# Kernel tuning notes

Measured on AMD Instinct MI355X. Metric: run time of the kernel, lower is better.

Reference implementation:

```python
import jax, jax.numpy as jnp
import numpy as np

DIM = 3072      # model dim (Qwen-Image)
HEADS = 24
HD = 128        # head dim; inner = HEADS*HD = 3072
INNER = HEADS * HD
FF = 4 * DIM    # 12288
S_IMG = 1024
S_TXT = 256
S_TOT = S_IMG + S_TXT
B = 1
EPS = 1e-6
SCALE_SHIFT = 1.0


def setup_inputs() -> dict:
    key = jax.random.key(0)
    ks = iter(jax.random.split(key, 64))
    W = 0.02

    def nrm(shape, s=W):
        return jax.random.normal(next(ks), shape, dtype=jnp.float32) * s

    # RoPE tables for the joint (txt first, then img) sequence, interleaved layout
    pos = jnp.arange(S_TOT, dtype=jnp.float32)
    inv = 1.0 / (10000.0 ** (jnp.arange(HD // 2, dtype=jnp.float32) / (HD // 2)))
    ang = pos[:, None] * inv[None, :]                       # [S, HD/2]
    rope_cos = jnp.repeat(jnp.cos(ang), 2, axis=-1)         # [S, HD]
    rope_sin = jnp.repeat(jnp.sin(ang), 2, axis=-1)

    inp = {
        "hidden_states": jax.random.normal(next(ks), (B, S_IMG, DIM), dtype=jnp.float32),
        "encoder_hidden_states": jax.random.normal(next(ks), (B, S_TXT, DIM), dtype=jnp.float32),
        "temb": jax.random.normal(next(ks), (B, DIM), dtype=jnp.float32),
        "rope_cos": rope_cos,
        "rope_sin": rope_sin,
        # modulation (AWQW4A16Linear equivalent)
        "img_mod_w": nrm((6 * DIM, DIM)), "img_mod_b": nrm((6 * DIM,)),
        "txt_mod_w": nrm((6 * DIM, DIM)), "txt_mod_b": nrm((6 * DIM,)),
        # attention (SVDQW4A4Linear equivalents)
        "qkv_w": nrm((3 * INNER, DIM)), "qkv_b": nrm((3 * INNER,)),
        "add_qkv_w": nrm((3 * INNER, DIM)), "add_qkv_b": nrm((3 * INNER,)),
        "norm_q_g": jnp.ones((HD,), jnp.float32), "norm_k_g": jnp.ones((HD,), jnp.float32),
        "norm_added_q_g": jnp.ones((HD,), jnp.float32), "norm_added_k_g": jnp.ones((HD,), jnp.float32),
        "to_out_w": nrm((DIM, INNER)), "to_out_b": nrm((DIM,)),
        "to_add_out_w": nrm((DIM, INNER)), "to_add_out_b": nrm((DIM,)),
        # MLPs
        "img_mlp_w1": nrm((FF, DIM)), "img_mlp_b1": nrm((FF,)),
        "img_mlp_w2": nrm((DIM, FF)), "img_mlp_b2": nrm((DIM,)),
        "txt_mlp_w1": nrm((FF, DIM)), "txt_mlp_b1": nrm((FF,)),
        "txt_mlp_w2": nrm((DIM, FF)), "txt_mlp_b2": nrm((DIM,)),
    }
    return inp


def _lin(x, w, b):
    return jnp.matmul(x, w.T) + b


def _ln(x):  # LayerNorm, no affine, eps=1e-6
    mu = jnp.mean(x, axis=-1, keepdims=True)
    var = jnp.mean(jnp.square(x - mu), axis=-1, keepdims=True)
    return (x - mu) * jax.lax.rsqrt(var + EPS)


def _rms(x, g):  # per-head RMSNorm over last dim (HD)
    ms = jnp.mean(jnp.square(x), axis=-1, keepdims=True)
    return x * jax.lax.rsqrt(ms + EPS) * g


def _rope(x, cos, sin):  # x: [B,S,H,D], cos/sin: [S,D], interleaved rotate
    x1 = x[..., 0::2]
    x2 = x[..., 1::2]
    xr = jnp.stack([-x2, x1], axis=-1).reshape(x.shape)
    return x * cos[None, :, None, :] + xr * sin[None, :, None, :]


def _reorder_mod(m):
    # view(B,-1,6).transpose(1,2).reshape(B,-1): de-interleave 6 modulation vecs
    b = m.shape[0]
    return m.reshape(b, DIM, 6).transpose(0, 2, 1).reshape(b, 6 * DIM)


def _modulate(x, mod):
    shift, scale, gate = jnp.split(mod, 3, axis=-1)
    return x * (scale + SCALE_SHIFT)[:, None, :] + shift[:, None, :], gate[:, None, :]


def _mlp(x, w1, b1, w2, b2):  # GELU(tanh) MLP
    h = jax.nn.gelu(_lin(x, w1, b1), approximate=True)
    return _lin(h, w2, b2)


def reference(hidden_states, encoder_hidden_states, temb, rope_cos, rope_sin,
              img_mod_w, img_mod_b, txt_mod_w, txt_mod_b,
              qkv_w, qkv_b, add_qkv_w, add_qkv_b,
              norm_q_g, norm_k_g, norm_added_q_g, norm_added_k_g,
              to_out_w, to_out_b, to_add_out_w, to_add_out_b,
              img_mlp_w1, img_mlp_b1, img_mlp_w2, img_mlp_b2,
              txt_mlp_w1, txt_mlp_b1, txt_mlp_w2, txt_mlp_b2):
    b = hidden_states.shape[0]

    img_mod = _reorder_mod(_lin(jax.nn.silu(temb), img_mod_w, img_mod_b))
    txt_mod = _reorder_mod(_lin(jax.nn.silu(temb), txt_mod_w, txt_mod_b))
    img_mod1, img_mod2 = jnp.split(img_mod, 2, axis=-1)
    txt_mod1, txt_mod2 = jnp.split(txt_mod, 2, axis=-1)

    img_modulated, img_gate1 = _modulate(_ln(hidden_states), img_mod1)
    txt_modulated, txt_gate1 = _modulate(_ln(encoder_hidden_states), txt_mod1)

    # ---- joint attention ----
    img_q, img_k, img_v = jnp.split(_lin(img_modulated, qkv_w, qkv_b), 3, axis=-1)
    txt_q, txt_k, txt_v = jnp.split(_lin(txt_modulated, add_qkv_w, add_qkv_b), 3, axis=-1)

    def heads(x):  # [B,S,INNER] -> [B,S,H,HD]
        return x.reshape(b, x.shape[1], HEADS, HD)

    img_q = _rms(heads(img_q), norm_q_g)
    img_k = _rms(heads(img_k), norm_k_g)
    txt_q = _rms(heads(txt_q), norm_added_q_g)
    txt_k = _rms(heads(txt_k), norm_added_k_g)

    q = jnp.concatenate([txt_q, img_q], axis=1)  # txt first
    k = jnp.concatenate([txt_k, img_k], axis=1)
    v = jnp.concatenate([heads(txt_v), heads(img_v)], axis=1)

    q = _rope(q, rope_cos, rope_sin)
    k = _rope(k, rope_cos, rope_sin)

    scale = 1.0 / jnp.sqrt(jnp.float32(HD))
    scores = jnp.einsum('bqhd,bkhd->bhqk', q, k) * scale
    probs = jax.nn.softmax(scores, axis=-1)
    attn = jnp.einsum('bhqk,bkhd->bqhd', probs, v).reshape(b, S_TOT, INNER)

    txt_attn = attn[:, :S_TXT, :]
    img_attn = attn[:, S_TXT:, :]
    img_attn = _lin(img_attn, to_out_w, to_out_b)
    txt_attn = _lin(txt_attn, to_add_out_w, to_add_out_b)

    hidden_states = hidden_states + img_gate1 * img_attn
    encoder_hidden_states = encoder_hidden_states + txt_gate1 * txt_attn

    # ---- MLPs ----
    img_m2, img_gate2 = _modulate(_ln(hidden_states), img_mod2)
    hidden_states = hidden_states + img_gate2 * _mlp(img_m2, img_mlp_w1, img_mlp_b1, img_mlp_w2, img_mlp_b2)

    txt_m2, txt_gate2 = _modulate(_ln(encoder_hidden_states), txt_mod2)
    encoder_hidden_states = encoder_hidden_states + txt_gate2 * _mlp(txt_m2, txt_mlp_w1, txt_mlp_b1, txt_mlp_w2, txt_mlp_b2)

    return (encoder_hidden_states, hidden_states)
```

## Files before the change

### kernel.cpp

```cpp
#include <hip/hip_runtime.h>

#define DIMC   3072
#define HEADS  24
#define HD     128
#define FF     12288
#define S_IMG  1024
#define S_TXT  256
#define S_TOT  1280
#define EPSF   1e-6f

typedef __attribute__((ext_vector_type(8))) short bf16x8;
typedef __attribute__((ext_vector_type(4))) float f32x4;
typedef __attribute__((ext_vector_type(4))) float float4v;
typedef __attribute__((ext_vector_type(4))) unsigned int u32x4;

__device__ __forceinline__ unsigned short f2bf(float f) {
    union { float f; unsigned u; } c; c.f = f;
    unsigned u = c.u;
    unsigned r = (u + 0x7fffu + ((u >> 16) & 1u)) >> 16;
    return (unsigned short)r;
}
__device__ __forceinline__ float b2f(unsigned short h) {
    union { unsigned u; float f; } c; c.u = ((unsigned)h) << 16;
    return c.f;
}
__device__ __forceinline__ unsigned packbf(float a, float b) {
    union { float f; unsigned u; } x, y; x.f = a; y.f = b;
    return __builtin_amdgcn_perm(y.u + 0x8000u, x.u + 0x8000u, 0x07060302);
}
__device__ __forceinline__ float gelu_tanh(float v) {
    float u = 1.5957691216057308f * (v + 0.044715f * v * v * v);
    float e = __expf(u);
    float t = 1.0f - 2.0f / (e + 1.0f);
    return 0.5f * v * (1.0f + t);
}

#define GLL16(gsrc, ldst)                                                     \
    __builtin_amdgcn_global_load_lds(                                         \
        (const __attribute__((address_space(1))) void*)(gsrc),                \
        (__attribute__((address_space(3))) void*)(ldst), 16, 0, 0)

struct GemmArgs {
    const unsigned short* A;
    const void* B;
    const float* bias;
    void* out;
    const float* base;
    const float* gate;
};

__device__ __forceinline__ void epi_store(int EPI, const GemmArgs& g,
                                          float v, long o, int) {
}

template<int EPI>
__global__ __launch_bounds__(512, 2)
void gemm_big(GemmArgs g0, GemmArgs g1, int ysplit,
              int K, int lda, int ldb, int ldout)
{
    __shared__ __align__(16) char smem[131072];
    char* smemA = smem;
    char* smemB = smem + 65536;

    const int tid  = threadIdx.x;
    const int lane = tid & 63;
    const int wave = tid >> 6;
    const int wm = wave >> 2, wc = wave & 3;

    const int by = blockIdx.y;
    const bool second = (by >= ysplit);
    const GemmArgs g = second ? g1 : g0;
    const int bm = (second ? by - ysplit : by) * 256;
    const int bn = blockIdx.x * 256;

    const unsigned short* A = g.A;
    const float* Bf = (const float*)g.B;

    const int rA = lane >> 3;
    const int cA = (lane & 7) ^ rA;
    const int pB = tid & 7;
    const int rB0 = tid >> 3;
    const int swB = (rB0 & 7) << 4;

    float4v breg[4][2];

    auto BLOAD = [&](int t) {
        const float* src = Bf + (long)t * 64 + pB * 8;
        #pragma unroll
        for (int i = 0; i < 4; i++) {
            const float* p = src + (long)(bn + rB0 + i * 64) * ldb;
            breg[i][0] = *(const float4v*)p;
            breg[i][1] = *(const float4v*)(p + 4);
        }
    };
    auto ASTAGE = [&](int buf, int t) {
        const long kof = (long)t * 64 + cA * 8;
        #pragma unroll
        for (int i = 0; i < 4; i++) {
            int r = i * 64 + wave * 8 + rA;
            GLL16(A + (long)(bm + r) * lda + kof,
                  smemA + buf * 32768 + i * 8192 + wave * 1024);
        }
    };
    auto BSTORE = [&](int buf) {
        #pragma unroll
        for (int i = 0; i < 4; i++) {
            int r = rB0 + i * 64;
            u32x4 w;
            w[0] = packbf(breg[i][0][0], breg[i][0][1]);
            w[1] = packbf(breg[i][0][2], breg[i][0][3]);
            w[2] = packbf(breg[i][1][0], breg[i][1][1]);
            w[3] = packbf(breg[i][1][2], breg[i][1][3]);
            *(u32x4*)(smemB + buf * 32768 + r * 128 + ((pB * 16) ^ swB)) = w;
        }
    };

    f32x4 acc[8][4] = {};
    auto COMPUTE = [&](int buf) {
        #pragma unroll
        for (int ks = 0; ks < 2; ks++) {
            const int kb = ks * 64 + (lane >> 4) * 16;
            bf16x8 af[8], bfr[4];
            #pragma unroll
            for (int mi = 0; mi < 8; mi++) {
                int r = wm * 128 + mi * 16 + (lane & 15);
                af[mi] = *(const bf16x8*)(smemA + buf * 32768 + r * 128 + (kb ^ ((r & 7) << 4)));
            }
            #pragma unroll
            for (int ni = 0; ni < 4; ni++) {
                int r = wc * 64 + ni * 16 + (lane & 15);
                bfr[ni] = *(const bf16x8*)(smemB + buf * 32768 + r * 128 + (kb ^ ((r & 7) << 4)));
            }
            #pragma unroll
            for (int mi = 0; mi < 8; mi++)
                #pragma unroll
                for (int ni = 0; ni < 4; ni++)
                    acc[mi][ni] = __builtin_amdgcn_mfma_f32_16x16x32_bf16(
                        af[mi], bfr[ni], acc[mi][ni], 0, 0, 0);
        }
    };

    const int nk = K >> 6;
    BLOAD(0);
    ASTAGE(0, 0);
    BSTORE(0);
    __syncthreads();
    for (int t = 0; t < nk; ++t) {
        const int cur = t & 1;
        if (t + 1 < nk) {
            BLOAD(t + 1);
            ASTAGE(cur ^ 1, t + 1);
        }
        __builtin_amdgcn_sched_barrier(0);
        COMPUTE(cur);
        __builtin_amdgcn_sched_barrier(0);
        if (t + 1 < nk) BSTORE(cur ^ 1);
        __syncthreads();
    }

    unsigned short* outh = (unsigned short*)g.out;
    float*          outf = (float*)g.out;
    #pragma unroll
    for (int mi = 0; mi < 8; mi++) {
        #pragma unroll
        for (int ni = 0; ni < 4; ni++) {
            int n = bn + wc * 64 + ni * 16 + (lane & 15);
            float bv = g.bias ? g.bias[n] : 0.0f;
            #pragma unroll
            for (int r = 0; r < 4; r++) {
                int m = bm + wm * 128 + mi * 16 + (lane >> 4) * 4 + r;
                float v = acc[mi][ni][r] + bv;
                long o = (long)m * ldout + n;
                if constexpr (EPI == 0) outf[o] = v;
                else                    outh[o] = f2bf(gelu_tanh(v));
            }
        }
    }
}

template<int EPI, bool BF16B>
__global__ __launch_bounds__(256)
void gemm_bt(GemmArgs g0, GemmArgs g1, int ysplit,
             int K, int lda, int ldb, int ldout,
             long batchA, long batchB, long batchOut)
{
    __shared__ __align__(16) char smem[65536];
    char* smemA = smem;
    char* smemB = smem + 32768;

    const int tid  = threadIdx.x;
    const int lane = tid & 63;
    const int wave = tid >> 6;
    const int wm = wave >> 1, wc = wave & 1;

    const int by = blockIdx.y;
    const bool second = (by >= ysplit);
    const GemmArgs g = second ? g1 : g0;
    const int bm = (second ? by - ysplit : by) * 128;
    const int bn = blockIdx.x * 128;

    const unsigned short* A = g.A + (long)blockIdx.z * batchA;
    const float* Bf = (const float*)g.B + (long)blockIdx.z * batchB;
    const unsigned short* Bh = (const unsigned short*)g.B + (long)blockIdx.z * batchB;

    const int rA = lane >> 3;
    const int cA = (lane & 7) ^ rA;
    const int pB = tid & 7;
    const int rB0 = tid >> 3;
    const int swB = (rB0 & 7) << 4;

    float4v breg[4][2];

    auto BLOAD = [&](int t) {
        const float* src = Bf + (long)t * 64 + pB * 8;
        #pragma unroll
        for (int i = 0; i < 4; i++) {
            const float* p = src + (long)(bn + rB0 + i * 32) * ldb;
            breg[i][0] = *(const float4v*)p;
            breg[i][1] = *(const float4v*)(p + 4);
        }
    };
    auto STAGE_A = [&](int buf, int t) {
        const long kof = (long)t * 64 + cA * 8;
        #pragma unroll
        for (int i = 0; i < 4; i++) {
            int r = i * 32 + wave * 8 + rA;
            GLL16(A + (long)(bm + r) * lda + kof,
                  smemA + buf * 16384 + i * 4096 + wave * 1024);
        }
    };
    auto STAGE_B16 = [&](int buf, int t) {
        const long kof = (long)t * 64 + cA * 8;
        #pragma unroll
        for (int i = 0; i < 4; i++) {
            int r = i * 32 + wave * 8 + rA;
            GLL16(Bh + (long)(bn + r) * ldb + kof,
                  smemB + buf * 16384 + i * 4096 + wave * 1024);
        }
    };
    auto BSTORE = [&](int buf) {
        #pragma unroll
        for (int i = 0; i < 4; i++) {
            int r = rB0 + i * 32;
            u32x4 w;
            w[0] = packbf(breg[i][0][0], breg[i][0][1]);
            w[1] = packbf(breg[i][0][2], breg[i][0][3]);
            w[2] = packbf(breg[i][1][0], breg[i][1][1]);
            w[3] = packbf(breg[i][1][2], breg[i][1][3]);
            *(u32x4*)(smemB + buf * 16384 + r * 128 + ((pB * 16) ^ swB)) = w;
        }
    };

    f32x4 acc[4][4] = {};
    auto COMPUTE = [&](int buf) {
        #pragma unroll
        for (int ks = 0; ks < 2; ks++) {
            const int kb = ks * 64 + (lane >> 4) * 16;
            bf16x8 af[4], bfr[4];
            #pragma unroll
            for (int mi = 0; mi < 4; mi++) {
                int r = wm * 64 + mi * 16 + (lane & 15);
                af[mi] = *(const bf16x8*)(smemA + buf * 16384 + r * 128 + (kb ^ ((r & 7) << 4)));
            }
            #pragma unroll
            for (int ni = 0; ni < 4; ni++) {
                int r = wc * 64 + ni * 16 + (lane & 15);
                bfr[ni] = *(const bf16x8*)(smemB + buf * 16384 + r * 128 + (kb ^ ((r & 7) << 4)));
            }
            #pragma unroll
            for (int mi = 0; mi < 4; mi++)
                #pragma unroll
                for (int ni = 0; ni < 4; ni++)
                    acc[mi][ni] = __builtin_amdgcn_mfma_f32_16x16x32_bf16(
                        af[mi], bfr[ni], acc[mi][ni], 0, 0, 0);
        }
    };

    const int nk = K >> 6;
    if constexpr (BF16B) {
        STAGE_A(0, 0); STAGE_B16(0, 0);
    } else {
        BLOAD(0); STAGE_A(0, 0); BSTORE(0);
    }
    __syncthreads();
    for (int t = 0; t < nk; ++t) {
        const int cur = t & 1;
        if (t + 1 < nk) {
            if constexpr (BF16B) {
                STAGE_A(cur ^ 1, t + 1); STAGE_B16(cur ^ 1, t + 1);
            } else {
                BLOAD(t + 1); STAGE_A(cur ^ 1, t + 1);
            }
        }
        __builtin_amdgcn_sched_barrier(0);
        COMPUTE(cur);
        __builtin_amdgcn_sched_barrier(0);
        if constexpr (!BF16B) { if (t + 1 < nk) BSTORE(cur ^ 1); }
        __syncthreads();
    }

    unsigned short* outh = (unsigned short*)g.out + (long)blockIdx.z * batchOut;
    float*          outf = (float*)g.out + (long)blockIdx.z * batchOut;
    #pragma unroll
    for (int mi = 0; mi < 4; mi++) {
        #pragma unroll
        for (int ni = 0; ni < 4; ni++) {
            int n = bn + wc * 64 + ni * 16 + (lane & 15);
            float bv = g.bias ? g.bias[n] : 0.0f;
            #pragma unroll
            for (int r = 0; r < 4; r++) {
                int m = bm + wm * 64 + mi * 16 + (lane >> 4) * 4 + r;
                float v = acc[mi][ni][r] + bv;
                long o = (long)m * ldout + n;
                if constexpr (EPI == 0)      outf[o] = v;
                else if constexpr (EPI == 1) outh[o] = f2bf(v);
                else if constexpr (EPI == 2) outh[o] = f2bf(gelu_tanh(v));
                else                         outf[o] = g.base[o] + g.gate[n] * v;
            }
        }
    }
}

__global__ void silu_k(const float* __restrict__ x, float* __restrict__ out) {
    int i = blockIdx.x * 256 + threadIdx.x;
    if (i < DIMC) { float v = x[i]; out[i] = v / (1.0f + expf(-v)); }
}

__global__ __launch_bounds__(256)
void mod_gemv(const float* __restrict__ st,
              const float* __restrict__ Wimg, const float* __restrict__ bimg,
              const float* __restrict__ Wtxt, const float* __restrict__ btxt,
              float* __restrict__ mimg, float* __restrict__ mtxt)
{
    int wv = threadIdx.x >> 6, lane = threadIdx.x & 63;
    int r = blockIdx.x * 4 + wv;
    const float* W = blockIdx.y ? Wtxt : Wimg;
    const float* b = blockIdx.y ? btxt : bimg;
    float* out = blockIdx.y ? mtxt : mimg;
    const float* row = W + (long)r * DIMC;
    float acc = 0.f;
    #pragma unroll
    for (int j = 0; j < 12; j++) {
        float4v wvv = ((const float4v*)row)[lane + j * 64];
        float4v xv  = ((const float4v*)st)[lane + j * 64];
        acc += wvv[0] * xv[0] + wvv[1] * xv[1] + wvv[2] * xv[2] + wvv[3] * xv[3];
    }
    #pragma unroll
    for (int o = 32; o; o >>= 1) acc += __shfl_xor(acc, o);
    if (lane == 0) {
        int d = r / 6, j6 = r % 6;
        out[j6 * DIMC + d] = acc + b[r];
    }
}

__global__ __launch_bounds__(256)
void ln_mod(const float* __restrict__ x, const float* __restrict__ shift,
            const float* __restrict__ scale, unsigned short* __restrict__ out)
{
    __shared__ float red[8];
    long row = blockIdx.x;
    const float* xr = x + row * DIMC;
    float4v v[3];
    float sum = 0.f, sq = 0.f;
    #pragma unroll
    for (int j = 0; j < 3; j++) {
        v[j] = ((const float4v*)xr)[threadIdx.x + j * 256];
        #pragma unroll
        for (int c = 0; c < 4; c++) { sum += v[j][c]; sq += v[j][c] * v[j][c]; }
    }
    int lane = threadIdx.x & 63, wv = threadIdx.x >> 6;
    #pragma unroll
    for (int o = 32; o; o >>= 1) { sum += __shfl_xor(sum, o); sq += __shfl_xor(sq, o); }
    if (lane == 0) { red[wv] = sum; red[4 + wv] = sq; }
    __syncthreads();
    sum = red[0] + red[1] + red[2] + red[3];
    sq  = red[4] + red[5] + red[6] + red[7];
    float mu = sum / DIMC;
    float var = sq / DIMC - mu * mu;
    float rstd = rsqrtf(var + EPSF);
    #pragma unroll
    for (int j = 0; j < 3; j++) {
        int nb = (threadIdx.x + j * 256) * 4;
        #pragma unroll
        for (int c = 0; c < 4; c++) {
            int n = nb + c;
            float y = (v[j][c] - mu) * rstd * (scale[n] + 1.0f) + shift[n];
            out[row * DIMC + n] = f2bf(y);
        }
    }
}

__global__ __launch_bounds__(64)
void qkv_post(const float* __restrict__ qkv_img, const float* __restrict__ qkv_txt,
              const float* __restrict__ nqg, const float* __restrict__ nkg,
              const float* __restrict__ naqg, const float* __restrict__ nakg,
              const float* __restrict__ rc, const float* __restrict__ rs,
              unsigned short* __restrict__ q, unsigned short* __restrict__ k,
              unsigned short* __restrict__ vt)
{
    int s = blockIdx.x;
    int h = blockIdx.y;
    int d0 = threadIdx.x;
    const float *src, *gq, *gk;
    if (s < S_TXT) { src = qkv_txt + (long)s * 3 * DIMC; gq = naqg; gk = nakg; }
    else           { src = qkv_img + (long)(s - S_TXT) * 3 * DIMC; gq = nqg; gk = nkg; }

    float q0 = src[h * HD + d0],            q1 = src[h * HD + d0 + 64];
    float k0 = src[DIMC + h * HD + d0],     k1 = src[DIMC + h * HD + d0 + 64];
    float v0 = src[2 * DIMC + h * HD + d0], v1 = src[2 * DIMC + h * HD + d0 + 64];

    float sqq = q0 * q0 + q1 * q1;
    float sqk = k0 * k0 + k1 * k1;
    #pragma unroll
    for (int o = 32; o; o >>= 1) { sqq += __shfl_xor(sqq, o); sqk += __shfl_xor(sqk, o); }
    float rq = rsqrtf(sqq / (float)HD + EPSF);
    float rk = rsqrtf(sqk / (float)HD + EPSF);
    q0 *= rq * gq[d0]; q1 *= rq * gq[d0 + 64];
    k0 *= rk * gk[d0]; k1 *= rk * gk[d0 + 64];

    float qp0 = __shfl_xor(q0, 1), qp1 = __shfl_xor(q1, 1);
    float kp0 = __shfl_xor(k0, 1), kp1 = __shfl_xor(k1, 1);
    float c0 = rc[(long)s * HD + d0], c1 = rc[(long)s * HD + d0 + 64];
    float s0 = rs[(long)s * HD + d0], s1 = rs[(long)s * HD + d0 + 64];
    float sgn = (d0 & 1) ? 1.0f : -1.0f;
    float qo0 = q0 * c0 + sgn * qp0 * s0;
    float qo1 = q1 * c1 + sgn * qp1 * s1;
    float ko0 = k0 * c0 + sgn * kp0 * s0;
    float ko1 = k1 * c1 + sgn * kp1 * s1;

    const float scl = 0.08838834764831845f;
    long qkbase = ((long)h * S_TOT + s) * HD;
    q[qkbase + d0]      = f2bf(qo0 * scl);
    q[qkbase + d0 + 64] = f2bf(qo1 * scl);
    k[qkbase + d0]      = f2bf(ko0);
    k[qkbase + d0 + 64] = f2bf(ko1);
    vt[((long)h * HD + d0) * S_TOT + s]        = f2bf(v0);
    vt[((long)h * HD + d0 + 64) * S_TOT + s]   = f2bf(v1);
}

__global__ __launch_bounds__(256)
void softmax_k(unsigned short* __restrict__ scores)
{
    long row = (long)blockIdx.x * 4 + (threadIdx.x >> 6);
    int lane = threadIdx.x & 63;
    unsigned short* p = scores + row * S_TOT;
    float v[20];
    float mx = -1e30f;
    #pragma unroll
    for (int j = 0; j < 20; j++) { v[j] = b2f(p[lane + j * 64]); mx = fmaxf(mx, v[j]); }
    #pragma unroll
    for (int o = 32; o; o >>= 1) mx = fmaxf(mx, __shfl_xor(mx, o));
    float sum = 0.f;
    #pragma unroll
    for (int j = 0; j < 20; j++) { v[j] = __expf(v[j] - mx); sum += v[j]; }
    #pragma unroll
    for (int o = 32; o; o >>= 1) sum += __shfl_xor(sum, o);
    float inv = 1.0f / sum;
    #pragma unroll
    for (int j = 0; j < 20; j++) p[lane + j * 64] = f2bf(v[j] * inv);
}

extern "C" void kernel_launch(void* const* d_in, const int* in_sizes, int n_in,
                              void* d_out, int out_size, void* d_ws, size_t ws_size,
                              hipStream_t stream)
{
    const float* hidden   = (const float*)d_in[0];
    const float* enc      = (const float*)d_in[1];
    const float* temb     = (const float*)d_in[2];
    const float* rope_cos = (const float*)d_in[3];
    const float* rope_sin = (const float*)d_in[4];
    const float* img_mod_w = (const float*)d_in[5];
    const float* img_mod_b = (const float*)d_in[6];
    const float* txt_mod_w = (const float*)d_in[7];
    const float* txt_mod_b = (const float*)d_in[8];
    const float* qkv_w     = (const float*)d_in[9];
    const float* qkv_b     = (const float*)d_in[10];
    const float* add_qkv_w = (const float*)d_in[11];
    const float* add_qkv_b = (const float*)d_in[12];
    const float* norm_q_g  = (const float*)d_in[13];
    const float* norm_k_g  = (const float*)d_in[14];
    const float* norm_aq_g = (const float*)d_in[15];
    const float* norm_ak_g = (const float*)d_in[16];
    const float* to_out_w  = (const float*)d_in[17];
    const float* to_out_b  = (const float*)d_in[18];
    const float* to_add_out_w = (const float*)d_in[19];
    const float* to_add_out_b = (const float*)d_in[20];
    const float* img_mlp_w1 = (const float*)d_in[21];
    const float* img_mlp_b1 = (const float*)d_in[22];
    const float* img_mlp_w2 = (const float*)d_in[23];
    const float* img_mlp_b2 = (const float*)d_in[24];
    const float* txt_mlp_w1 = (const float*)d_in[25];
    const float* txt_mlp_b1 = (const float*)d_in[26];
    const float* txt_mlp_w2 = (const float*)d_in[27];
    const float* txt_mlp_b2 = (const float*)d_in[28];

    char* w = (char*)d_ws;
    auto alloc = [&](size_t bytes) { char* p = w; w += (bytes + 255) & ~(size_t)255; return p; };
    float* silu_t  = (float*)alloc(DIMC * 4);
    float* mod_img = (float*)alloc(6 * DIMC * 4);
    float* mod_txt = (float*)alloc(6 * DIMC * 4);
    unsigned short* mA_img = (unsigned short*)alloc((long)S_IMG * DIMC * 2);
    unsigned short* mA_txt = (unsigned short*)alloc((long)S_TXT * DIMC * 2);
    float* qkv_img = (float*)alloc((long)S_IMG * 3 * DIMC * 4);
    float* qkv_txt = (float*)alloc((long)S_TXT * 3 * DIMC * 4);
    unsigned short* qb = (unsigned short*)alloc((long)HEADS * S_TOT * HD * 2);
    unsigned short* kb = (unsigned short*)alloc((long)HEADS * S_TOT * HD * 2);
    unsigned short* vt = (unsigned short*)alloc((long)HEADS * HD * S_TOT * 2);
    unsigned short* scores = (unsigned short*)alloc((long)HEADS * S_TOT * S_TOT * 2);
    unsigned short* attn = (unsigned short*)alloc((long)S_TOT * DIMC * 2);
    float* h1_img = (float*)alloc((long)S_IMG * DIMC * 4);
    float* h1_txt = (float*)alloc((long)S_TXT * DIMC * 4);
    unsigned short* gelu_img = (unsigned short*)alloc((long)S_IMG * FF * 2);
    unsigned short* gelu_txt = (unsigned short*)alloc((long)S_TXT * FF * 2);

    float* out_enc = (float*)d_out;
    float* out_hid = (float*)d_out + (long)S_TXT * DIMC;

    silu_k<<<12, 256, 0, stream>>>(temb, silu_t);
    mod_gemv<<<dim3(4608, 2), 256, 0, stream>>>(silu_t, img_mod_w, img_mod_b,
                                                txt_mod_w, txt_mod_b, mod_img, mod_txt);

    ln_mod<<<S_IMG, 256, 0, stream>>>(hidden, mod_img, mod_img + DIMC, mA_img);
    ln_mod<<<S_TXT, 256, 0, stream>>>(enc, mod_txt, mod_txt + DIMC, mA_txt);

    {
        GemmArgs gi{mA_img, qkv_w, qkv_b, qkv_img, nullptr, nullptr};
        GemmArgs gt{mA_txt, add_qkv_w, add_qkv_b, qkv_txt, nullptr, nullptr};
        gemm_big<0><<<dim3(36, 5), 512, 0, stream>>>(
            gi, gt, 4, DIMC, DIMC, DIMC, 3 * DIMC);
    }

    qkv_post<<<dim3(S_TOT, HEADS), 64, 0, stream>>>(
        qkv_img, qkv_txt, norm_q_g, norm_k_g, norm_aq_g, norm_ak_g,
        rope_cos, rope_sin, qb, kb, vt);

    {
        GemmArgs gs{qb, kb, nullptr, scores, nullptr, nullptr};
        gemm_bt<1, true><<<dim3(10, 10, HEADS), 256, 0, stream>>>(
            gs, gs, 10, HD, HD, HD, S_TOT,
            (long)S_TOT * HD, (long)S_TOT * HD, (long)S_TOT * S_TOT);
    }
    softmax_k<<<(HEADS * S_TOT) / 4, 256, 0, stream>>>(scores);
    {
        GemmArgs gp{scores, vt, nullptr, attn, nullptr, nullptr};
        gemm_bt<1, true><<<dim3(1, 10, HEADS), 256, 0, stream>>>(
            gp, gp, 10, S_TOT, S_TOT, S_TOT, DIMC,
            (long)S_TOT * S_TOT, (long)HD * S_TOT, HD);
    }

    {
        GemmArgs gi{attn + (long)S_TXT * DIMC, to_out_w, to_out_b, h1_img, hidden, mod_img + 2 * DIMC};
        GemmArgs gt{attn, to_add_out_w, to_add_out_b, h1_txt, enc, mod_txt + 2 * DIMC};
        gemm_bt<3, false><<<dim3(24, 10), 256, 0, stream>>>(
            gi, gt, 8, DIMC, DIMC, DIMC, DIMC, 0, 0, 0);
    }

    ln_mod<<<S_IMG, 256, 0, stream>>>(h1_img, mod_img + 3 * DIMC, mod_img + 4 * DIMC, mA_img);
    ln_mod<<<S_TXT, 256, 0, stream>>>(h1_txt, mod_txt + 3 * DIMC, mod_txt + 4 * DIMC, mA_txt);

    {
        GemmArgs gi{mA_img, img_mlp_w1, img_mlp_b1, gelu_img, nullptr, nullptr};
        GemmArgs gt{mA_txt, txt_mlp_w1, txt_mlp_b1, gelu_txt, nullptr, nullptr};
        gemm_big<2><<<dim3(48, 5), 512, 0, stream>>>(
            gi, gt, 4, DIMC, DIMC, DIMC, FF);
    }
    {
        GemmArgs gi{gelu_img, img_mlp_w2, img_mlp_b2, out_hid, h1_img, mod_img + 5 * DIMC};
        GemmArgs gt{gelu_txt, txt_mlp_w2, txt_mlp_b2, out_enc, h1_txt, mod_txt + 5 * DIMC};
        gemm_bt<3, false><<<dim3(24, 10), 256, 0, stream>>>(
            gi, gt, 8, FF, FF, FF, DIMC, 0, 0, 0);
    }
}
```

Baseline: 863.6 us.

## Split-K the output and MLP-down GEMMs, fuse reduction with residual and LayerNorm

The to_out and MLP-down GEMMs, which ran on only 240 workgroups, are now split along K (2-way and 4-way) using the blockIdx.z batch dimension. Each split writes fp32 partials into the reused scores buffer. New reduce_ln and reduce_out kernels sum the partials and apply bias, gate and residual; reduce_ln also performs the following LayerNorm and modulation, which replaces the separate ln_mod launches. The aim is better GPU occupancy on the narrow GEMMs, at the cost of extra partial-buffer traffic.

```diff
diff --git a/kernel.cpp b/kernel.cpp
--- a/kernel.cpp
+++ b/kernel.cpp
@@ -45,13 +45,8 @@
     const void* B;
     const float* bias;
     void* out;
-    const float* base;
-    const float* gate;
+    long bOut;
 };
-
-__device__ __forceinline__ void epi_store(int EPI, const GemmArgs& g,
-                                          float v, long o, int) {
-}
 
 template<int EPI>
 __global__ __launch_bounds__(512, 2)
@@ -182,7 +177,7 @@
 __global__ __launch_bounds__(256)
 void gemm_bt(GemmArgs g0, GemmArgs g1, int ysplit,
              int K, int lda, int ldb, int ldout,
-             long batchA, long batchB, long batchOut)
+             long batchA, long batchB)
 {
     __shared__ __align__(16) char smem[65536];
     char* smemA = smem;
@@ -299,8 +294,8 @@
         __syncthreads();
     }
 
-    unsigned short* outh = (unsigned short*)g.out + (long)blockIdx.z * batchOut;
-    float*          outf = (float*)g.out + (long)blockIdx.z * batchOut;
+    unsigned short* outh = (unsigned short*)g.out + (long)blockIdx.z * g.bOut;
+    float*          outf = (float*)g.out + (long)blockIdx.z * g.bOut;
     #pragma unroll
     for (int mi = 0; mi < 4; mi++) {
         #pragma unroll
@@ -313,9 +308,7 @@
                 float v = acc[mi][ni][r] + bv;
                 long o = (long)m * ldout + n;
                 if constexpr (EPI == 0)      outf[o] = v;
-                else if constexpr (EPI == 1) outh[o] = f2bf(v);
-                else if constexpr (EPI == 2) outh[o] = f2bf(gelu_tanh(v));
-                else                         outf[o] = g.base[o] + g.gate[n] * v;
+                else                         outh[o] = f2bf(v);
             }
         }
     }
@@ -388,6 +381,75 @@
             out[row * DIMC + n] = f2bf(y);
         }
     }
+}
+
+__global__ __launch_bounds__(256)
+void reduce_ln(const float* __restrict__ p0, const float* __restrict__ p1,
+               const float* __restrict__ pbias, const float* __restrict__ base,
+               const float* __restrict__ gate1, const float* __restrict__ shift2,
+               const float* __restrict__ scale2,
+               float* __restrict__ h1, unsigned short* __restrict__ mA)
+{
+    __shared__ float red[8];
+    long off = (long)blockIdx.x * DIMC;
+    float4v v[3];
+    float sum = 0.f, sq = 0.f;
+    #pragma unroll
+    for (int j = 0; j < 3; j++) {
+        int idx = threadIdx.x + j * 256;
+        float4v a  = ((const float4v*)(base + off))[idx];
+        float4v q0 = ((const float4v*)(p0 + off))[idx];
+        float4v q1 = ((const float4v*)(p1 + off))[idx];
+        float4v gb = ((const float4v*)pbias)[idx];
+        float4v gt = ((const float4v*)gate1)[idx];
+        #pragma unroll
+        for (int c = 0; c < 4; c++) {
+            float val = a[c] + gt[c] * (gb[c] + q0[c] + q1[c]);
+            v[j][c] = val; sum += val; sq += val * val;
+        }
+        ((float4v*)(h1 + off))[idx] = v[j];
+    }
+    int lane = threadIdx.x & 63, wv = threadIdx.x >> 6;
+    #pragma unroll
+    for (int o = 32; o; o >>= 1) { sum += __shfl_xor(sum, o); sq += __shfl_xor(sq, o); }
+    if (lane == 0) { red[wv] = sum; red[4 + wv] = sq; }
+    __syncthreads();
+    sum = red[0] + red[1] + red[2] + red[3];
+    sq  = red[4] + red[5] + red[6] + red[7];
+    float mu = sum / DIMC;
+    float rstd = rsqrtf(sq / DIMC - mu * mu + EPSF);
+    #pragma unroll
+    for (int j = 0; j < 3; j++) {
+        int nb = (threadIdx.x + j * 256) * 4;
+        #pragma unroll
+        for (int c = 0; c < 4; c++) {
+            int n = nb + c;
+            float y = (v[j][c] - mu) * rstd * (scale2[n] + 1.0f) + shift2[n];
+            mA[off + n] = f2bf(y);
+        }
+    }
+}
+
+__global__ __launch_bounds__(256)
+void reduce_out(const float* __restrict__ p, long PS,
+                const float* __restrict__ h1, const float* __restrict__ wbias,
+                const float* __restrict__ gate2, float* __restrict__ out, int n4)
+{
+    int i = blockIdx.x * 256 + threadIdx.x;
+    if (i >= n4) return;
+    int n = (i * 4) % DIMC;
+    float4v s = ((const float4v*)p)[i];
+    float4v s1 = ((const float4v*)(p + PS))[i];
+    float4v s2 = ((const float4v*)(p + 2 * PS))[i];
+    float4v s3 = ((const float4v*)(p + 3 * PS))[i];
+    float4v h = ((const float4v*)h1)[i];
+    float4v bv = *(const float4v*)(wbias + n);
+    float4v gv = *(const float4v*)(gate2 + n);
+    float4v r;
+    #pragma unroll
+    for (int c = 0; c < 4; c++)
+        r[c] = h[c] + gv[c] * (bv[c] + s[c] + s1[c] + s2[c] + s3[c]);
+    ((float4v*)out)[i] = r;
 }
 
 __global__ __launch_bounds__(64)
@@ -513,6 +575,11 @@
     unsigned short* gelu_img = (unsigned short*)alloc((long)S_IMG * FF * 2);
     unsigned short* gelu_txt = (unsigned short*)alloc((long)S_TXT * FF * 2);
 
+    const long PS = (long)S_TOT * DIMC;
+    float* part = (float*)scores;
+    float* part_img = part;
+    float* part_txt = part + (long)S_IMG * DIMC;
+
     float* out_enc = (float*)d_out;
     float* out_hid = (float*)d_out + (long)S_TXT * DIMC;
 
@@ -524,8 +591,8 @@
     ln_mod<<<S_TXT, 256, 0, stream>>>(enc, mod_txt, mod_txt + DIMC, mA_txt);
 
     {
-        GemmArgs gi{mA_img, qkv_w, qkv_b, qkv_img, nullptr, nullptr};
-        GemmArgs gt{mA_txt, add_qkv_w, add_qkv_b, qkv_txt, nullptr, nullptr};
+        GemmArgs gi{mA_img, qkv_w, qkv_b, qkv_img, 0};
+        GemmArgs gt{mA_txt, add_qkv_w, add_qkv_b, qkv_txt, 0};
         gemm_big<0><<<dim3(36, 5), 512, 0, stream>>>(
             gi, gt, 4, DIMC, DIMC, DIMC, 3 * DIMC);
     }
@@ -535,39 +602,52 @@
         rope_cos, rope_sin, qb, kb, vt);
 
     {
-        GemmArgs gs{qb, kb, nullptr, scores, nullptr, nullptr};
+        GemmArgs gs{qb, kb, nullptr, scores, (long)S_TOT * S_TOT};
         gemm_bt<1, true><<<dim3(10, 10, HEADS), 256, 0, stream>>>(
             gs, gs, 10, HD, HD, HD, S_TOT,
-            (long)S_TOT * HD, (long)S_TOT * HD, (long)S_TOT * S_TOT);
+            (long)S_TOT * HD, (long)S_TOT * HD);
     }
     softmax_k<<<(HEADS * S_TOT) / 4, 256, 0, stream>>>(scores);
     {
-        GemmArgs gp{scores, vt, nullptr, attn, nullptr, nullptr};
+        GemmArgs gp{scores, vt, nullptr, attn, HD};
         gemm_bt<1, true><<<dim3(1, 10, HEADS), 256, 0, stream>>>(
             gp, gp, 10, S_TOT, S_TOT, S_TOT, DIMC,
-            (long)S_TOT * S_TOT, (long)HD * S_TOT, HD);
+            (long)S_TOT * S_TOT, (long)HD * S_TOT);
     }
 
     {
-        GemmArgs gi{attn + (long)S_TXT * DIMC, to_out_w, to_out_b, h1_img, hidden, mod_img + 2 * DIMC};
-        GemmArgs gt{attn, to_add_out_w, to_add_out_b, h1_txt, enc, mod_txt + 2 * DIMC};
-        gemm_bt<3, false><<<dim3(24, 10), 256, 0, stream>>>(
-            gi, gt, 8, DIMC, DIMC, DIMC, DIMC, 0, 0, 0);
-    }
-
-    ln_mod<<<S_IMG, 256, 0, stream>>>(h1_img, mod_img + 3 * DIMC, mod_img + 4 * DIMC, mA_img);
-    ln_mod<<<S_TXT, 256, 0, stream>>>(h1_txt, mod_txt + 3 * DIMC, mod_txt + 4 * DIMC, mA_txt);
+        GemmArgs gi{attn + (long)S_TXT * DIMC, to_out_w, nullptr, part_img, PS};
+        GemmArgs gt{attn, to_add_out_w, nullptr, part_txt, PS};
+        gemm_bt<0, false><<<dim3(24, 10, 2), 256, 0, stream>>>(
+            gi, gt, 8, 1536, DIMC, DIMC, DIMC, 1536, 1536);
+    }
+
+    reduce_ln<<<S_IMG, 256, 0, stream>>>(
+        part_img, part_img + PS, to_out_b, hidden,
+        mod_img + 2 * DIMC, mod_img + 3 * DIMC, mod_img + 4 * DIMC,
+        h1_img, mA_img);
+    reduce_ln<<<S_TXT, 256, 0, stream>>>(
+        part_txt, part_txt + PS, to_add_out_b, enc,
+        mod_txt + 2 * DIMC, mod_txt + 3 * DIMC, mod_txt + 4 * DIMC,
+        h1_txt, mA_txt);
 
     {
-        GemmArgs gi{mA_img, img_mlp_w1, img_mlp_b1, gelu_img, nullptr, nullptr};
-        GemmArgs gt{mA_txt, txt_mlp_w1, txt_mlp_b1, gelu_txt, nullptr, nullptr};
+        GemmArgs gi{mA_img, img_mlp_w1, img_mlp_b1, gelu_img, 0};
+        GemmArgs gt{mA_txt, txt_mlp_w1, txt_mlp_b1, gelu_txt, 0};
         gemm_big<2><<<dim3(48, 5), 512, 0, stream>>>(
             gi, gt, 4, DIMC, DIMC, DIMC, FF);
     }
+
     {
-        GemmArgs gi{gelu_img, img_mlp_w2, img_mlp_b2, out_hid, h1_img, mod_img + 5 * DIMC};
-        GemmArgs gt{gelu_txt, txt_mlp_w2, txt_mlp_b2, out_enc, h1_txt, mod_txt + 5 * DIMC};
-        gemm_bt<3, false><<<dim3(24, 10), 256, 0, stream>>>(
-            gi, gt, 8, FF, FF, FF, DIMC, 0, 0, 0);
-    }
-}
+        GemmArgs gi{gelu_img, img_mlp_w2, nullptr, part_img, PS};
+        GemmArgs gt{gelu_txt, txt_mlp_w2, nullptr, part_txt, PS};
+        gemm_bt<0, false><<<dim3(24, 10, 4), 256, 0, stream>>>(
+            gi, gt, 8, 3072, FF, FF, DIMC, 3072, 3072);
+    }
+    reduce_out<<<(S_IMG * DIMC / 4 + 255) / 256, 256, 0, stream>>>(
+        part_img, PS, h1_img, img_mlp_b2, mod_img + 5 * DIMC, out_hid,
+        S_IMG * DIMC / 4);
+    reduce_out<<<(S_TXT * DIMC / 4 + 255) / 256, 256, 0, stream>>>(
+        part_txt, PS, h1_txt, txt_mlp_b2, mod_txt + 5 * DIMC, out_enc,
+        S_TXT * DIMC / 4);
+}
```

Result: faster. 765.0 us (-11.4%).
